# Kernel optimization log

Hardware: AMD Instinct MI355X
Metric: run time of the kernel (lower is better)

Reference implementation:

```python
import jax, jax.numpy as jnp
import numpy as np

B, S, D, H = 2, 2048, 1024, 16
DK = D // H


def setup_inputs() -> dict:
    key = jax.random.key(0)
    ks = jax.random.split(key, 11)
    s = 1.0 / np.sqrt(D)
    inp = {
        "q": jax.random.normal(ks[0], (B, S, D), jnp.float32),
        "k": jax.random.normal(ks[1], (B, S, D), jnp.float32),
        "v": jax.random.normal(ks[2], (B, S, D), jnp.float32),
        "mask": jnp.tril(jnp.ones((S, S), jnp.int32))[None, None],  # [1,1,S,S] causal
        "Wq": jax.random.normal(ks[3], (D, D), jnp.float32) * s,
        "bq": jnp.zeros((D,), jnp.float32),
        "Wk": jax.random.normal(ks[4], (D, D), jnp.float32) * s,
        "bk": jnp.zeros((D,), jnp.float32),
        "Wv": jax.random.normal(ks[5], (D, D), jnp.float32) * s,
        "bv": jnp.zeros((D,), jnp.float32),
        "Wo": jax.random.normal(ks[6], (D, D), jnp.float32) * s,
        "bo": jnp.zeros((D,), jnp.float32),
    }
    return inp


def reference(q, k, v, mask, Wq, bq, Wk, bk, Wv, bv, Wo, bo):
    # projections -> [B, H, S, DK]
    def split_heads(x):
        return x.reshape(B, S, H, DK).transpose(0, 2, 1, 3)

    Q = split_heads(q @ Wq + bq)
    K = split_heads(k @ Wk + bk)
    V = split_heads(v @ Wv + bv)

    scores = jnp.einsum("bhqd,bhkd->bhqk", Q, K) / jnp.sqrt(jnp.float32(DK))
    scores = jnp.where(mask == 0, jnp.float32(-1e9), scores)
    # source applies dropout(p=0.0) here -> identity
    attn = jax.nn.softmax(scores, axis=-1)  # [B,H,S,S]
    x = jnp.einsum("bhqk,bhkd->bhqd", attn, V)
    x = x.transpose(0, 2, 1, 3).reshape(B, S, D)
    return x @ Wo + bo
```

## Files before the change

### kernel.cpp

```cpp
#include <hip/hip_runtime.h>
#include <hip/hip_bf16.h>
#include <stdint.h>

#define Bb 2
#define Ss 2048
#define Dd 1024
#define Hh 16
#define DKk 64

#define QSCALE 0.180336878f

typedef __attribute__((ext_vector_type(8))) short s8v;
typedef __attribute__((ext_vector_type(4))) short s4v;
typedef __attribute__((ext_vector_type(4))) float f4v;
typedef __attribute__((ext_vector_type(16))) float f16v;

#if __has_builtin(__builtin_amdgcn_exp2f)
#define EXP2(x) __builtin_amdgcn_exp2f(x)
#else
#define EXP2(x) __expf((x)*0.69314718f)
#endif

__device__ __forceinline__ unsigned short f2bf(float f) {
    __hip_bfloat16 h = __float2bfloat16(f);
    union { __hip_bfloat16 h; unsigned short u; } c; c.h = h;
    return c.u;
}

__device__ __forceinline__ unsigned pack_bf2(float lo, float hi) {
    __hip_bfloat162 h = __float22bfloat162_rn(float2{lo, hi});
    union { __hip_bfloat162 h; unsigned u; } c; c.h = h;
    return c.u;
}

__device__ __forceinline__ void gload16(const void* g, void* l) {
    __builtin_amdgcn_global_load_lds((__attribute__((address_space(1))) void*)g,
                                     (__attribute__((address_space(3))) void*)l, 16, 0, 0);
}

__global__ void __launch_bounds__(256) prep_x(const float* __restrict__ q,
                                              const float* __restrict__ k,
                                              const float* __restrict__ v,
                                              unsigned short* __restrict__ xq,
                                              unsigned short* __restrict__ xk,
                                              unsigned short* __restrict__ xv) {
    const int z = blockIdx.z;
    const float* s = (z == 0) ? q : ((z == 1) ? k : v);
    unsigned short* d = (z == 0) ? xq : ((z == 1) ? xk : xv);
    long i = ((long)blockIdx.x * blockDim.x + threadIdx.x) * 8;
    f4v a = *(const f4v*)(s + i);
    f4v b = *(const f4v*)(s + i + 4);
    union { unsigned u[4]; s8v v; } o;
    o.u[0] = pack_bf2(a[0], a[1]);
    o.u[1] = pack_bf2(a[2], a[3]);
    o.u[2] = pack_bf2(b[0], b[1]);
    o.u[3] = pack_bf2(b[2], b[3]);
    *(s8v*)(void*)(d + i) = o.v;
}

__global__ void __launch_bounds__(256) prep_w(const float* __restrict__ Wq,
                                              const float* __restrict__ Wk,
                                              const float* __restrict__ Wv,
                                              const float* __restrict__ Wo,
                                              unsigned short* __restrict__ o0,
                                              unsigned short* __restrict__ o1,
                                              unsigned short* __restrict__ o2,
                                              unsigned short* __restrict__ o3) {
    __shared__ float t[64][65];
    const int z = blockIdx.z;
    const float* W = (z == 0) ? Wq : ((z == 1) ? Wk : ((z == 2) ? Wv : Wo));
    unsigned short* O = (z == 0) ? o0 : ((z == 1) ? o1 : ((z == 2) ? o2 : o3));
    const int n0 = (blockIdx.x & 15) * 64;
    const int k0 = (blockIdx.x >> 4) * 64;
    const int c = threadIdx.x & 63;
    const int r4 = threadIdx.x >> 6;
#pragma unroll
    for (int i = 0; i < 16; i++) {
        int r = i * 4 + r4;
        t[r][c] = W[(long)(k0 + r) * Dd + n0 + c];
    }
    __syncthreads();
#pragma unroll
    for (int i = 0; i < 16; i++) {
        int r = i * 4 + r4;
        O[(long)(n0 + r) * Dd + k0 + c] = f2bf(t[c][r]);
    }
}

template <int MODE>
__device__ __forceinline__ void gemm_body(const unsigned short* __restrict__ A,
                                          const unsigned short* __restrict__ Bt,
                                          const float* __restrict__ bias,
                                          void* __restrict__ out, float oscale,
                                          unsigned short* smem, int m0, int n0) {
    unsigned short* As = smem;
    unsigned short* Bs = smem + 128 * 64;
    const int tid = threadIdx.x;
    const int l = tid & 63;
    const int w = tid >> 6;
    const int wr = w >> 1, wc = w & 1;
    const int lr = l & 15, lg = l >> 4;

    f4v acc[4][4];
#pragma unroll
    for (int m = 0; m < 4; m++)
#pragma unroll
        for (int n = 0; n < 4; n++) acc[m][n] = (f4v){0.f, 0.f, 0.f, 0.f};

    const int srow = tid >> 3;
    const int sg = (tid & 7) ^ (srow & 7);
    char* lbaseA = (char*)As + w * 1024;
    char* lbaseB = (char*)Bs + w * 1024;

#define STAGE_T(t_)                                                                    \
    do {                                                                               \
        const int k0_ = (t_) * 64;                                                     \
        _Pragma("unroll") for (int i_ = 0; i_ < 4; i_++) {                             \
            int rowA_ = i_ * 32 + srow;                                                \
            gload16((const char*)A + ((long)(m0 + rowA_) * 1024 + k0_) * 2 + sg * 16,  \
                    lbaseA + i_ * 4096);                                               \
            gload16((const char*)Bt + ((long)(n0 + rowA_) * 1024 + k0_) * 2 + sg * 16, \
                    lbaseB + i_ * 4096);                                               \
        }                                                                              \
    } while (0)

    STAGE_T(0);
    for (int t = 0; t < 16; t++) {
        asm volatile("s_waitcnt vmcnt(0)" ::: "memory");
        __builtin_amdgcn_s_barrier();
        __builtin_amdgcn_sched_barrier(0);

        s8v af[2][4], bfr[2][4];
#pragma unroll
        for (int kk = 0; kk < 2; kk++) {
#pragma unroll
            for (int m = 0; m < 4; m++) {
                int row = wr * 64 + m * 16 + lr;
                int gc = (kk * 4 + lg) ^ (row & 7);
                af[kk][m] = *(const s8v*)((const char*)As + row * 128 + gc * 16);
            }
#pragma unroll
            for (int n = 0; n < 4; n++) {
                int row = wc * 64 + n * 16 + lr;
                int gc = (kk * 4 + lg) ^ (row & 7);
                bfr[kk][n] = *(const s8v*)((const char*)Bs + row * 128 + gc * 16);
            }
        }
        asm volatile("s_waitcnt lgkmcnt(0)" ::: "memory");
        __builtin_amdgcn_sched_barrier(0);
        __builtin_amdgcn_s_barrier();
        __builtin_amdgcn_sched_barrier(0);

        if (t + 1 < 16) STAGE_T(t + 1);

#pragma unroll
        for (int kk = 0; kk < 2; kk++)
#pragma unroll
            for (int m = 0; m < 4; m++)
#pragma unroll
                for (int n = 0; n < 4; n++)
                    acc[m][n] = __builtin_amdgcn_mfma_f32_16x16x32_bf16(
                        af[kk][m], bfr[kk][n], acc[m][n], 0, 0, 0);
    }
#undef STAGE_T

#pragma unroll
    for (int n = 0; n < 4; n++) {
        int col = n0 + wc * 64 + n * 16 + lr;
        float bv = bias[col];
#pragma unroll
        for (int m = 0; m < 4; m++) {
#pragma unroll
            for (int r = 0; r < 4; r++) {
                int row = m0 + wr * 64 + m * 16 + lg * 4 + r;
                float val = acc[m][n][r] + bv;
                if (MODE == 0) {
                    int b = row >> 11, s2 = row & 2047, h = col >> 6, d = col & 63;
                    ((unsigned short*)out)[(((b * Hh + h) * Ss + s2) << 6) + d] =
                        f2bf(val * oscale);
                } else if (MODE == 1) {
                    int b = row >> 11, s2 = row & 2047, h = col >> 6, d = col & 63;
                    ((unsigned short*)out)[((b * Hh + h) * DKk + d) * Ss + s2] = f2bf(val);
                } else {
                    ((float*)out)[(long)row * Dd + col] = val;
                }
            }
        }
    }
}

__device__ __forceinline__ void xcd_tile(int bid, int& m0, int& n0) {
    int content = (bid & 7) * 32 + (bid >> 3);
    n0 = (content & 7) * 128;
    m0 = (content >> 3) * 128;
}

__global__ void __launch_bounds__(256) qkv_gemm(const unsigned short* __restrict__ xq,
                                                const unsigned short* __restrict__ xk,
                                                const unsigned short* __restrict__ xv,
                                                const unsigned short* __restrict__ Wqt,
                                                const unsigned short* __restrict__ Wkt,
                                                const unsigned short* __restrict__ Wvt,
                                                const float* __restrict__ bq,
                                                const float* __restrict__ bk,
                                                const float* __restrict__ bv,
                                                unsigned short* __restrict__ Qh,
                                                unsigned short* __restrict__ Kh,
                                                unsigned short* __restrict__ Vt) {
    __shared__ unsigned short smem[128 * 64 * 2];
    int m0, n0;
    xcd_tile(blockIdx.x, m0, n0);
    const int z = blockIdx.z;
    if (z == 0)
        gemm_body<0>(xq, Wqt, bq, Qh, QSCALE, smem, m0, n0);
    else if (z == 1)
        gemm_body<0>(xk, Wkt, bk, Kh, 1.f, smem, m0, n0);
    else
        gemm_body<1>(xv, Wvt, bv, Vt, 1.f, smem, m0, n0);
}

__global__ void __launch_bounds__(256) out_gemm(const unsigned short* __restrict__ x,
                                                const unsigned short* __restrict__ Wot,
                                                const float* __restrict__ bo,
                                                float* __restrict__ out) {
    __shared__ unsigned short smem[128 * 64 * 2];
    int m0, n0;
    xcd_tile(blockIdx.x, m0, n0);
    gemm_body<2>(x, Wot, bo, out, 1.f, smem, m0, n0);
}

__global__ void __launch_bounds__(256) attn_kernel(const unsigned short* __restrict__ Qh,
                                                   const unsigned short* __restrict__ Kh,
                                                   const unsigned short* __restrict__ Vt,
                                                   unsigned short* __restrict__ xatt) {
    __shared__ __align__(16) char ldsbuf[32768];
    unsigned short* Ks = (unsigned short*)ldsbuf;
    unsigned short* Vs = (unsigned short*)(ldsbuf + 16384);
    const int tid = threadIdx.x;
    const int w = tid >> 6, l = tid & 63;
    const int lq = l & 31;
    const int hi = l >> 5;
    const int bh = blockIdx.x & 31;
    const int tile = 63 - (blockIdx.x >> 5);
    const int q0 = tile * 32;
    const int b = bh >> 4, h = bh & 15;
    const unsigned short* Qp = Qh + bh * Ss * DKk;
    const unsigned short* Kp = Kh + bh * Ss * DKk;
    const unsigned short* Vp = Vt + bh * DKk * Ss;

    s8v qf[4];
#pragma unroll
    for (int kk = 0; kk < 4; kk++)
        qf[kk] = *(const s8v*)(Qp + (q0 + lq) * 64 + kk * 16 + hi * 8);

    f16v oT0, oT1;
#pragma unroll
    for (int r = 0; r < 16; r++) { oT0[r] = 0.f; oT1[r] = 0.f; }
    float mx = -1e30f, sm = 0.f;
    const int nkb = tile + 1;
    const int nch = (nkb + 3) >> 2;

#define STAGE_CH(ch_)                                                          \
    do {                                                                       \
        const int kv0_ = (ch_) * 128;                                          \
        _Pragma("unroll") for (int i_ = 0; i_ < 4; i_++) {                     \
            const int G0_ = i_ * 256 + w * 64;                                 \
            int G_ = G0_ + l;                                                  \
            int row_ = G_ >> 3, gd_ = G_ & 7;                                  \
            int gs_ = gd_ ^ (row_ & 7);                                        \
            gload16(Kp + (kv0_ + row_) * 64 + gs_ * 8, (char*)Ks + G0_ * 16);  \
        }                                                                      \
        _Pragma("unroll") for (int i_ = 0; i_ < 4; i_++) {                     \
            const int G0_ = i_ * 256 + w * 64;                                 \
            int G_ = G0_ + l;                                                  \
            int row_ = G_ >> 4, gd_ = G_ & 15;                                 \
            int gs_ = gd_ ^ (row_ & 15);                                       \
            gload16(Vp + (long)row_ * Ss + kv0_ + gs_ * 8, (char*)Vs + G0_ * 16); \
        }                                                                      \
    } while (0)

    STAGE_CH(0);
    for (int ch = 0; ch < nch; ch++) {
        asm volatile("s_waitcnt vmcnt(0)" ::: "memory");
        __builtin_amdgcn_s_barrier();
        __builtin_amdgcn_sched_barrier(0);

        s8v kf[4], vf0[2], vf1[2];
#pragma unroll
        for (int kk = 0; kk < 4; kk++) {
            int row = w * 32 + lq;
            int g = (2 * kk + hi) ^ (row & 7);
            kf[kk] = *(const s8v*)((const char*)Ks + (row * 8 + g) * 16);
        }
#pragma unroll
        for (int kk = 0; kk < 2; kk++) {
            int g0 = 4 * w + 2 * kk + hi;
            vf0[kk] = *(const s8v*)((const char*)Vs + (lq * 16 + (g0 ^ (lq & 15))) * 16);
            vf1[kk] =
                *(const s8v*)((const char*)Vs + ((32 + lq) * 16 + (g0 ^ (lq & 15))) * 16);
        }
        asm volatile("s_waitcnt lgkmcnt(0)" ::: "memory");
        __builtin_amdgcn_sched_barrier(0);
        __builtin_amdgcn_s_barrier();
        __builtin_amdgcn_sched_barrier(0);

        if (ch + 1 < nch) STAGE_CH(ch + 1);

        const int kb = ch * 4 + w;
        if (kb < nkb) {
            const int k0 = kb * 32;
            f16v S;
#pragma unroll
            for (int r = 0; r < 16; r++) S[r] = 0.f;
#pragma unroll
            for (int kk = 0; kk < 4; kk++)
                S = __builtin_amdgcn_mfma_f32_32x32x16_bf16(kf[kk], qf[kk], S, 0, 0, 0);

            const bool diag = (kb == nkb - 1);
            float e[16];
#pragma unroll
            for (int r = 0; r < 16; r++) {
                float v = S[r];
                if (diag) {
                    int kv = k0 + (r & 3) + 8 * (r >> 2) + 4 * hi;
                    if (kv > q0 + lq) v = -1e30f;
                }
                e[r] = v;
            }
            float m8[8];
#pragma unroll
            for (int i = 0; i < 8; i++) m8[i] = fmaxf(e[i], e[i + 8]);
#pragma unroll
            for (int i = 0; i < 4; i++) m8[i] = fmaxf(m8[i], m8[i + 4]);
            float pmax = fmaxf(fmaxf(m8[0], m8[1]), fmaxf(m8[2], m8[3]));
            pmax = fmaxf(pmax, __shfl_xor(pmax, 32));

            if (!__all(pmax - mx <= 8.f)) {
                float mn = fmaxf(mx, pmax);
                float sc = EXP2(mx - mn);
                mx = mn;
                sm *= sc;
#pragma unroll
                for (int r = 0; r < 16; r++) { oT0[r] *= sc; oT1[r] *= sc; }
            }
#pragma unroll
            for (int r = 0; r < 16; r++) e[r] = EXP2(e[r] - mx);
            float s8s[8];
#pragma unroll
            for (int i = 0; i < 8; i++) s8s[i] = e[i] + e[i + 8];
#pragma unroll
            for (int i = 0; i < 4; i++) s8s[i] = s8s[i] + s8s[i + 4];
            float rs = (s8s[0] + s8s[1]) + (s8s[2] + s8s[3]);
            sm += rs + __shfl_xor(rs, 32);

            unsigned pk[8], sw[8];
#pragma unroll
            for (int i = 0; i < 8; i++) pk[i] = pack_bf2(e[2 * i], e[2 * i + 1]);
#pragma unroll
            for (int i = 0; i < 8; i++) sw[i] = (unsigned)__shfl_xor((int)pk[i], 32);
            union { unsigned u[4]; s8v v; } p0, p1;
            p0.u[0] = hi ? sw[2] : pk[0];
            p0.u[1] = hi ? sw[3] : pk[1];
            p0.u[2] = hi ? pk[2] : sw[0];
            p0.u[3] = hi ? pk[3] : sw[1];
            p1.u[0] = hi ? sw[6] : pk[4];
            p1.u[1] = hi ? sw[7] : pk[5];
            p1.u[2] = hi ? pk[6] : sw[4];
            p1.u[3] = hi ? pk[7] : sw[5];

            oT0 = __builtin_amdgcn_mfma_f32_32x32x16_bf16(vf0[0], p0.v, oT0, 0, 0, 0);
            oT0 = __builtin_amdgcn_mfma_f32_32x32x16_bf16(vf0[1], p1.v, oT0, 0, 0, 0);
            oT1 = __builtin_amdgcn_mfma_f32_32x32x16_bf16(vf1[0], p0.v, oT1, 0, 0, 0);
            oT1 = __builtin_amdgcn_mfma_f32_32x32x16_bf16(vf1[1], p1.v, oT1, 0, 0, 0);
        }
    }
#undef STAGE_CH

    float(*plds)[64][34] = (float(*)[64][34])ldsbuf;
    if (w >= 2) {
        float* p = plds[w - 2][l];
        p[0] = mx; p[1] = sm;
#pragma unroll
        for (int r = 0; r < 16; r++) { p[2 + r] = oT0[r]; p[18 + r] = oT1[r]; }
    }
    __syncthreads();
    if (w < 2) {
        const float* p = plds[w][l];
        float m2 = p[0], s2 = p[1];
        float M = fmaxf(mx, m2);
        float a = EXP2(mx - M), bb = EXP2(m2 - M);
        sm = sm * a + s2 * bb;
#pragma unroll
        for (int r = 0; r < 16; r++) {
            oT0[r] = oT0[r] * a + p[2 + r] * bb;
            oT1[r] = oT1[r] * a + p[18 + r] * bb;
        }
        mx = M;
    }
    __syncthreads();
    if (w == 1) {
        float* p = plds[0][l];
        p[0] = mx; p[1] = sm;
#pragma unroll
        for (int r = 0; r < 16; r++) { p[2 + r] = oT0[r]; p[18 + r] = oT1[r]; }
    }
    __syncthreads();
    if (w != 0) return;
    {
        const float* p = plds[0][l];
        float m2 = p[0], s2 = p[1];
        float M = fmaxf(mx, m2);
        float a = EXP2(mx - M), bb = EXP2(m2 - M);
        sm = sm * a + s2 * bb;
#pragma unroll
        for (int r = 0; r < 16; r++) {
            oT0[r] = oT0[r] * a + p[2 + r] * bb;
            oT1[r] = oT1[r] * a + p[18 + r] * bb;
        }
    }

    const float inv = 1.f / sm;
    const int q = q0 + lq;
    unsigned short* orow = xatt + (long)(b * Ss + q) * Dd + h * 64;
#pragma unroll
    for (int g = 0; g < 4; g++) {
        union { unsigned u[2]; s4v v; } v0, v1;
        v0.u[0] = pack_bf2(oT0[g * 4 + 0] * inv, oT0[g * 4 + 1] * inv);
        v0.u[1] = pack_bf2(oT0[g * 4 + 2] * inv, oT0[g * 4 + 3] * inv);
        v1.u[0] = pack_bf2(oT1[g * 4 + 0] * inv, oT1[g * 4 + 1] * inv);
        v1.u[1] = pack_bf2(oT1[g * 4 + 2] * inv, oT1[g * 4 + 3] * inv);
        int d = 8 * g + 4 * hi;
        *(s4v*)(orow + d) = v0.v;
        *(s4v*)(orow + 32 + d) = v1.v;
    }
}

extern "C" void kernel_launch(void* const* d_in, const int* in_sizes, int n_in,
                              void* d_out, int out_size, void* d_ws, size_t ws_size,
                              hipStream_t stream) {
    const float* q  = (const float*)d_in[0];
    const float* k  = (const float*)d_in[1];
    const float* v  = (const float*)d_in[2];
    const float* Wq = (const float*)d_in[4];
    const float* bq = (const float*)d_in[5];
    const float* Wk = (const float*)d_in[6];
    const float* bk = (const float*)d_in[7];
    const float* Wv = (const float*)d_in[8];
    const float* bv = (const float*)d_in[9];
    const float* Wo = (const float*)d_in[10];
    const float* bo = (const float*)d_in[11];
    float* out = (float*)d_out;

    char* ws = (char*)d_ws;
    unsigned short* xq  = (unsigned short*)(ws + 0);
    unsigned short* xk  = (unsigned short*)(ws + 8388608);
    unsigned short* xv  = (unsigned short*)(ws + 16777216);
    unsigned short* Wqt = (unsigned short*)(ws + 25165824);
    unsigned short* Wkt = (unsigned short*)(ws + 27262976);
    unsigned short* Wvt = (unsigned short*)(ws + 29360128);
    unsigned short* Wot = (unsigned short*)(ws + 31457280);
    unsigned short* Qh  = (unsigned short*)(ws + 33554432);
    unsigned short* Kh  = (unsigned short*)(ws + 41943040);
    unsigned short* Vtp = (unsigned short*)(ws + 50331648);
    unsigned short* xat = (unsigned short*)(ws + 58720256);

    prep_x<<<dim3(2048, 1, 3), 256, 0, stream>>>(q, k, v, xq, xk, xv);
    prep_w<<<dim3(256, 1, 4), 256, 0, stream>>>(Wq, Wk, Wv, Wo, Wqt, Wkt, Wvt, Wot);
    qkv_gemm<<<dim3(256, 1, 3), 256, 0, stream>>>(xq, xk, xv, Wqt, Wkt, Wvt,
                                                  bq, bk, bv, Qh, Kh, Vtp);
    attn_kernel<<<dim3(2048), 256, 0, stream>>>(Qh, Kh, Vtp, xat);
    out_gemm<<<dim3(256), 256, 0, stream>>>(xat, Wot, bo, out);
}
```

Measured before the change: 133.4 us.

## Fuse fp32-to-bf16 input conversion into QKV GEMM tile loads

Removes the separate prep_x kernel that converted q, k and v from fp32 to bf16. The QKV GEMM now streams fp32 A tiles straight into LDS with an XOR swizzle over 16 groups and converts them to bf16 when it loads fragments. This drops a launch and a full read and write pass over the three 8 MB bf16 staging buffers. In exchange it doubles A-tile LDS traffic and footprint (48 KB per block), which may lower occupancy and adds conversion ALU work inside the main loop.

```diff
diff --git a/kernel.cpp b/kernel.cpp
--- a/kernel.cpp
+++ b/kernel.cpp
@@ -36,26 +36,6 @@
 __device__ __forceinline__ void gload16(const void* g, void* l) {
     __builtin_amdgcn_global_load_lds((__attribute__((address_space(1))) void*)g,
                                      (__attribute__((address_space(3))) void*)l, 16, 0, 0);
-}
-
-__global__ void __launch_bounds__(256) prep_x(const float* __restrict__ q,
-                                              const float* __restrict__ k,
-                                              const float* __restrict__ v,
-                                              unsigned short* __restrict__ xq,
-                                              unsigned short* __restrict__ xk,
-                                              unsigned short* __restrict__ xv) {
-    const int z = blockIdx.z;
-    const float* s = (z == 0) ? q : ((z == 1) ? k : v);
-    unsigned short* d = (z == 0) ? xq : ((z == 1) ? xk : xv);
-    long i = ((long)blockIdx.x * blockDim.x + threadIdx.x) * 8;
-    f4v a = *(const f4v*)(s + i);
-    f4v b = *(const f4v*)(s + i + 4);
-    union { unsigned u[4]; s8v v; } o;
-    o.u[0] = pack_bf2(a[0], a[1]);
-    o.u[1] = pack_bf2(a[2], a[3]);
-    o.u[2] = pack_bf2(b[0], b[1]);
-    o.u[3] = pack_bf2(b[2], b[3]);
-    *(s8v*)(void*)(d + i) = o.v;
 }
 
 __global__ void __launch_bounds__(256) prep_w(const float* __restrict__ Wq,
@@ -87,14 +67,14 @@
     }
 }
 
-template <int MODE>
-__device__ __forceinline__ void gemm_body(const unsigned short* __restrict__ A,
+template <int MODE, bool AF32>
+__device__ __forceinline__ void gemm_body(const void* __restrict__ Av,
                                           const unsigned short* __restrict__ Bt,
                                           const float* __restrict__ bias,
                                           void* __restrict__ out, float oscale,
-                                          unsigned short* smem, int m0, int n0) {
-    unsigned short* As = smem;
-    unsigned short* Bs = smem + 128 * 64;
+                                          char* smem, int m0, int n0) {
+    char* As = smem;
+    char* Bs = smem + (AF32 ? 32768 : 16384);
     const int tid = threadIdx.x;
     const int l = tid & 63;
     const int w = tid >> 6;
@@ -109,19 +89,36 @@
 
     const int srow = tid >> 3;
     const int sg = (tid & 7) ^ (srow & 7);
-    char* lbaseA = (char*)As + w * 1024;
-    char* lbaseB = (char*)Bs + w * 1024;
-
-#define STAGE_T(t_)                                                                    \
-    do {                                                                               \
-        const int k0_ = (t_) * 64;                                                     \
-        _Pragma("unroll") for (int i_ = 0; i_ < 4; i_++) {                             \
-            int rowA_ = i_ * 32 + srow;                                                \
-            gload16((const char*)A + ((long)(m0 + rowA_) * 1024 + k0_) * 2 + sg * 16,  \
-                    lbaseA + i_ * 4096);                                               \
-            gload16((const char*)Bt + ((long)(n0 + rowA_) * 1024 + k0_) * 2 + sg * 16, \
-                    lbaseB + i_ * 4096);                                               \
-        }                                                                              \
+    char* lbaseB = Bs + w * 1024;
+
+#define STAGE_T(t_)                                                                     \
+    do {                                                                                \
+        const int k0_ = (t_) * 64;                                                      \
+        if (AF32) {                                                                     \
+            const float* A32_ = (const float*)Av;                                       \
+            _Pragma("unroll") for (int i_ = 0; i_ < 8; i_++) {                          \
+                const int G0_ = i_ * 256 + w * 64;                                      \
+                int G_ = G0_ + l;                                                       \
+                int row_ = G_ >> 4, gd_ = G_ & 15;                                      \
+                int gs_ = gd_ ^ (row_ & 15);                                            \
+                gload16(A32_ + (long)(m0 + row_) * 1024 + k0_ + gs_ * 4,                \
+                        As + G0_ * 16);                                                 \
+            }                                                                           \
+        } else {                                                                        \
+            const unsigned short* A_ = (const unsigned short*)Av;                       \
+            char* lbaseA_ = As + w * 1024;                                              \
+            _Pragma("unroll") for (int i_ = 0; i_ < 4; i_++) {                          \
+                int rowA_ = i_ * 32 + srow;                                             \
+                gload16((const char*)A_ + ((long)(m0 + rowA_) * 1024 + k0_) * 2 +       \
+                            sg * 16,                                                    \
+                        lbaseA_ + i_ * 4096);                                           \
+            }                                                                           \
+        }                                                                               \
+        _Pragma("unroll") for (int i_ = 0; i_ < 4; i_++) {                              \
+            int rowA_ = i_ * 32 + srow;                                                 \
+            gload16((const char*)Bt + ((long)(n0 + rowA_) * 1024 + k0_) * 2 + sg * 16,  \
+                    lbaseB + i_ * 4096);                                                \
+        }                                                                               \
     } while (0)
 
     STAGE_T(0);
@@ -136,14 +133,27 @@
 #pragma unroll
             for (int m = 0; m < 4; m++) {
                 int row = wr * 64 + m * 16 + lr;
-                int gc = (kk * 4 + lg) ^ (row & 7);
-                af[kk][m] = *(const s8v*)((const char*)As + row * 128 + gc * 16);
+                if (AF32) {
+                    int g0 = kk * 8 + lg * 2;
+                    int s0 = g0 ^ (row & 15);
+                    f4v a0 = *(const f4v*)(As + (row * 16 + s0) * 16);
+                    f4v a1 = *(const f4v*)(As + (row * 16 + (s0 ^ 1)) * 16);
+                    union { unsigned u[4]; s8v v; } o;
+                    o.u[0] = pack_bf2(a0[0], a0[1]);
+                    o.u[1] = pack_bf2(a0[2], a0[3]);
+                    o.u[2] = pack_bf2(a1[0], a1[1]);
+                    o.u[3] = pack_bf2(a1[2], a1[3]);
+                    af[kk][m] = o.v;
+                } else {
+                    int gc = (kk * 4 + lg) ^ (row & 7);
+                    af[kk][m] = *(const s8v*)(As + row * 128 + gc * 16);
+                }
             }
 #pragma unroll
             for (int n = 0; n < 4; n++) {
                 int row = wc * 64 + n * 16 + lr;
                 int gc = (kk * 4 + lg) ^ (row & 7);
-                bfr[kk][n] = *(const s8v*)((const char*)Bs + row * 128 + gc * 16);
+                bfr[kk][n] = *(const s8v*)(Bs + row * 128 + gc * 16);
             }
         }
         asm volatile("s_waitcnt lgkmcnt(0)" ::: "memory");
@@ -195,9 +205,9 @@
     m0 = (content >> 3) * 128;
 }
 
-__global__ void __launch_bounds__(256) qkv_gemm(const unsigned short* __restrict__ xq,
-                                                const unsigned short* __restrict__ xk,
-                                                const unsigned short* __restrict__ xv,
+__global__ void __launch_bounds__(256) qkv_gemm(const float* __restrict__ q,
+                                                const float* __restrict__ k,
+                                                const float* __restrict__ v,
                                                 const unsigned short* __restrict__ Wqt,
                                                 const unsigned short* __restrict__ Wkt,
                                                 const unsigned short* __restrict__ Wvt,
@@ -207,26 +217,26 @@
                                                 unsigned short* __restrict__ Qh,
                                                 unsigned short* __restrict__ Kh,
                                                 unsigned short* __restrict__ Vt) {
-    __shared__ unsigned short smem[128 * 64 * 2];
+    __shared__ __align__(16) char smem[49152];
     int m0, n0;
     xcd_tile(blockIdx.x, m0, n0);
     const int z = blockIdx.z;
     if (z == 0)
-        gemm_body<0>(xq, Wqt, bq, Qh, QSCALE, smem, m0, n0);
+        gemm_body<0, true>(q, Wqt, bq, Qh, QSCALE, smem, m0, n0);
     else if (z == 1)
-        gemm_body<0>(xk, Wkt, bk, Kh, 1.f, smem, m0, n0);
+        gemm_body<0, true>(k, Wkt, bk, Kh, 1.f, smem, m0, n0);
     else
-        gemm_body<1>(xv, Wvt, bv, Vt, 1.f, smem, m0, n0);
+        gemm_body<1, true>(v, Wvt, bv, Vt, 1.f, smem, m0, n0);
 }
 
 __global__ void __launch_bounds__(256) out_gemm(const unsigned short* __restrict__ x,
                                                 const unsigned short* __restrict__ Wot,
                                                 const float* __restrict__ bo,
                                                 float* __restrict__ out) {
-    __shared__ unsigned short smem[128 * 64 * 2];
+    __shared__ __align__(16) char smem[32768];
     int m0, n0;
     xcd_tile(blockIdx.x, m0, n0);
-    gemm_body<2>(x, Wot, bo, out, 1.f, smem, m0, n0);
+    gemm_body<2, false>(x, Wot, bo, out, 1.f, smem, m0, n0);
 }
 
 __global__ void __launch_bounds__(256) attn_kernel(const unsigned short* __restrict__ Qh,
@@ -452,9 +462,6 @@
     float* out = (float*)d_out;
 
     char* ws = (char*)d_ws;
-    unsigned short* xq  = (unsigned short*)(ws + 0);
-    unsigned short* xk  = (unsigned short*)(ws + 8388608);
-    unsigned short* xv  = (unsigned short*)(ws + 16777216);
     unsigned short* Wqt = (unsigned short*)(ws + 25165824);
     unsigned short* Wkt = (unsigned short*)(ws + 27262976);
     unsigned short* Wvt = (unsigned short*)(ws + 29360128);
@@ -464,9 +471,8 @@
     unsigned short* Vtp = (unsigned short*)(ws + 50331648);
     unsigned short* xat = (unsigned short*)(ws + 58720256);
 
-    prep_x<<<dim3(2048, 1, 3), 256, 0, stream>>>(q, k, v, xq, xk, xv);
     prep_w<<<dim3(256, 1, 4), 256, 0, stream>>>(Wq, Wk, Wv, Wo, Wqt, Wkt, Wvt, Wot);
-    qkv_gemm<<<dim3(256, 1, 3), 256, 0, stream>>>(xq, xk, xv, Wqt, Wkt, Wvt,
+    qkv_gemm<<<dim3(256, 1, 3), 256, 0, stream>>>(q, k, v, Wqt, Wkt, Wvt,
                                                   bq, bk, bv, Qh, Kh, Vtp);
     attn_kernel<<<dim3(2048), 256, 0, stream>>>(Qh, Kh, Vtp, xat);
     out_gemm<<<dim3(256), 256, 0, stream>>>(xat, Wot, bo, out);
```

Measured after the change: 174.5 us. 30.8% more time.
